# Performance work log

Hardware: AMD Instinct MI355X
Metric: run time of the kernel (lower is better)

Reference implementation:

```python
import jax, jax.numpy as jnp
import numpy as np

B, NPG, DEG = 16, 2048, 16          # graphs, nodes per graph, avg degree
N_TOT = B * NPG
E_TOT = N_TOT * DEG
NEG_SLOPE = 0.2


def _gat(x, src, dst, n, w, a_src, a_dst, b):
    # PyG GATConv: concat heads, add self loops, leaky_relu(0.2), segment softmax over targets
    H, C = a_src.shape
    h = (x @ w.T).reshape(n, H, C)                       # [n,H,C]
    sl = jnp.arange(n, dtype=src.dtype)
    s = jnp.concatenate([src, sl])
    d = jnp.concatenate([dst, sl])
    e = jax.nn.leaky_relu((h * a_src).sum(-1)[s] + (h * a_dst).sum(-1)[d], NEG_SLOPE)  # [E+n,H]
    emax = jax.lax.stop_gradient(jax.ops.segment_max(e, d, num_segments=n))
    ee = jnp.exp(e - emax[d])
    alpha = ee / (jax.ops.segment_sum(ee, d, num_segments=n)[d] + 1e-16)
    out = jax.ops.segment_sum(alpha[:, :, None] * h[s], d, num_segments=n)  # [n,H,C]
    return out.reshape(n, H * C) + b


def _gcn(x, src, dst, mask, n, w, b):
    # PyG GCNConv with self loops + symmetric norm; mask = float edge validity
    h = x @ w.T
    deg = jax.ops.segment_sum(mask, dst, num_segments=n) + 1.0  # +1 for self loop
    dinv = jax.lax.rsqrt(deg)
    coef = dinv[src] * dinv[dst] * mask
    out = jax.ops.segment_sum(coef[:, None] * h[src], dst, num_segments=n) + (dinv * dinv)[:, None] * h
    return out + b


def _sag(x, src, dst, mask, b_graphs, npg, k, w_rel, b_rel, w_root):
    # PyG SAGPooling(ratio=0.5): GraphConv score, per-graph top-k, x[perm]*tanh(score[perm]), filter_adj
    n = b_graphs * npg
    agg = jax.ops.segment_sum(mask[:, None] * x[src], dst, num_segments=n)
    score = (agg @ w_rel.T + b_rel + x @ w_root.T)[:, 0]      # [n]
    _, idx = jax.lax.top_k(score.reshape(b_graphs, npg), k)    # [B,k]
    perm = (jnp.arange(b_graphs, dtype=jnp.int32)[:, None] * npg + idx).reshape(-1)
    x_new = x[perm] * jnp.tanh(score[perm])[:, None]
    new_id = jnp.full((n,), -1, jnp.int32).at[perm].set(jnp.arange(b_graphs * k, dtype=jnp.int32))
    ns, nd = new_id[src], new_id[dst]
    valid = mask * ((ns >= 0) & (nd >= 0)).astype(x.dtype)
    return x_new, jnp.maximum(ns, 0), jnp.maximum(nd, 0), valid


def setup_inputs() -> dict:
    key = jax.random.key(0)
    ks = jax.random.split(key, 32)

    def lin(k, o, i):
        return (jax.random.normal(k, (o, i), jnp.float32) / np.sqrt(i)).astype(jnp.float32)

    x = jax.random.normal(ks[0], (N_TOT, 64), jnp.float32)
    off = jnp.repeat(jnp.arange(B, dtype=jnp.int32) * NPG, NPG * DEG)
    src = off + jax.random.randint(ks[1], (E_TOT,), 0, NPG, jnp.int32)
    dst = off + jax.random.randint(ks[2], (E_TOT,), 0, NPG, jnp.int32)
    edge_index = jnp.stack([src, dst])
    batch = jnp.repeat(jnp.arange(B, dtype=jnp.int32), NPG)

    return {
        'x': x, 'edge_index': edge_index, 'batch': batch,
        'gat1_w': lin(ks[3], 256, 64), 'gat1_asrc': lin(ks[4], 4, 64), 'gat1_adst': lin(ks[5], 4, 64),
        'gat1_b': jnp.zeros((256,), jnp.float32),
        'gat2_w': lin(ks[6], 256, 256), 'gat2_asrc': lin(ks[7], 4, 64), 'gat2_adst': lin(ks[8], 4, 64),
        'gat2_b': jnp.zeros((256,), jnp.float32),
        # pooling GCN1: 256 -> 128
        'gcn1_w': lin(ks[9], 128, 256), 'gcn1_b': jnp.zeros((128,), jnp.float32),
        'sag1_wrel': lin(ks[10], 1, 128), 'sag1_brel': jnp.zeros((1,), jnp.float32), 'sag1_wroot': lin(ks[11], 1, 128),
        # pooling GCN2: 128 -> 128
        'gcn2_w': lin(ks[12], 128, 128), 'gcn2_b': jnp.zeros((128,), jnp.float32),
        'sag2_wrel': lin(ks[13], 1, 128), 'sag2_brel': jnp.zeros((1,), jnp.float32), 'sag2_wroot': lin(ks[14], 1, 128),
        # classifier 128 -> 256 -> 128 -> 10
        'fc1_w': lin(ks[15], 256, 128), 'fc1_b': jnp.zeros((256,), jnp.float32),
        'fc2_w': lin(ks[16], 128, 256), 'fc2_b': jnp.zeros((128,), jnp.float32),
        'out_w': lin(ks[17], 10, 128), 'out_b': jnp.zeros((10,), jnp.float32),
    }


def reference(x, edge_index, batch,
              gat1_w, gat1_asrc, gat1_adst, gat1_b,
              gat2_w, gat2_asrc, gat2_adst, gat2_b,
              gcn1_w, gcn1_b, sag1_wrel, sag1_brel, sag1_wroot,
              gcn2_w, gcn2_b, sag2_wrel, sag2_brel, sag2_wroot,
              fc1_w, fc1_b, fc2_w, fc2_b, out_w, out_b):
    n = x.shape[0]
    src, dst = edge_index[0], edge_index[1]
    ones = jnp.ones(src.shape[0], x.dtype)

    # GAT encoder
    h = jax.nn.relu(_gat(x, src, dst, n, gat1_w, gat1_asrc, gat1_adst, gat1_b))
    h = _gat(h, src, dst, n, gat2_w, gat2_asrc, gat2_adst, gat2_b)  # [n,256]

    # GCN + SAGPool x2
    h = jax.nn.relu(_gcn(h, src, dst, ones, n, gcn1_w, gcn1_b))
    k1 = NPG // 2
    h, s1, d1, m1 = _sag(h, src, dst, ones, B, NPG, k1, sag1_wrel, sag1_brel, sag1_wroot)
    h = jax.nn.relu(_gcn(h, s1, d1, m1, B * k1, gcn2_w, gcn2_b))
    k2 = k1 // 2
    h, s2, d2, m2 = _sag(h, s1, d1, m1, B, k1, k2, sag2_wrel, sag2_brel, sag2_wroot)

    # global mean pool (equal-size graphs -> simple reshape-mean; batch vec implied)
    g = h.reshape(B, k2, -1).mean(axis=1)  # [B,128]

    # classifier MLP
    g = jax.nn.relu(g @ fc1_w.T + fc1_b)
    g = jax.nn.relu(g @ fc2_w.T + fc2_b)
    return g @ out_w.T + out_b  # [B,10]
```

## Files before the change

kernel.cpp:

```cpp
#include <hip/hip_runtime.h>

#define N1 32768
#define EE 524288
#define NB 16
#define DEG 16
#define NPG1 2048
#define KK1 1024
#define N2 16384
#define NPG2 1024
#define KK2 512
#define N3 8192
#define CAP 64

typedef _Float16 half8_t __attribute__((ext_vector_type(8)));
typedef float floatx16 __attribute__((ext_vector_type(16)));

static __device__ __forceinline__ float leaky(float x){ return fmaxf(x, 0.2f*x); }

__global__ void scatter_split(const int* __restrict__ src, const int* __restrict__ dst,
                              int* __restrict__ cnt, int* __restrict__ esrc,
                              const float* __restrict__ w0, int n0,
                              const float* __restrict__ w1, int n1,
                              const float* __restrict__ w2, int n2,
                              const float* __restrict__ w3, int n3,
                              _Float16* __restrict__ wh, _Float16* __restrict__ wl){
    int b = blockIdx.x;
    int tid = threadIdx.x;
    if (b < EE/256){
        int i = b*256 + tid;
        int d = dst[i];
        int p = atomicAdd(&cnt[d], 1);
        esrc[(d << 6) + p] = src[i];
    } else {
        int i = (b - EE/256)*256 + tid;
        int n01 = n0 + n1, n012 = n01 + n2, nt = n012 + n3;
        if (i >= nt) return;
        float v = (i < n0) ? w0[i] : (i < n01) ? w1[i - n0] : (i < n012) ? w2[i - n01] : w3[i - n012];
        _Float16 h = (_Float16)v;
        wh[i] = h; wl[i] = (_Float16)(v - (float)h);
    }
}

__global__ void csr2_build(const int* __restrict__ perm, const int* __restrict__ nid,
                           const int* __restrict__ cnt, const int* __restrict__ EL,
                           int2* __restrict__ rpx2, float* __restrict__ dinv2,
                           int* __restrict__ EL2){
    int lane = threadIdx.x & 63;
    int w = threadIdx.x >> 6;
    int d2 = blockIdx.x*4 + w;
    int old = __builtin_amdgcn_readfirstlane(perm[d2]);
    int beg = old << 6;
    int end = beg + cnt[old];
    unsigned long long below = (1ull << lane) - 1ull;
    int c2 = 0;
    for (int i = beg; i < end; i += 64){
        int ii = i + lane;
        int sn = -1;
        if (ii < end) sn = nid[EL[ii]];
        bool take = sn >= 0;
        unsigned long long m = __ballot(take);
        int pos = c2 + __popcll(m & below);
        if (take) EL2[beg + pos] = sn;
        c2 += __popcll(m);
    }
    if (lane == 0){
        rpx2[d2] = make_int2(beg, beg + c2);
        dinv2[d2] = rsqrtf((float)c2 + 1.0f);
    }
}

#define KS 64
static __device__ __forceinline__ int ldsoff(int row, int k8){
    return row*64 + ((k8 ^ (row & 7)) << 3);
}

__global__ __launch_bounds__(256, 2) void gemm_h2(const float* __restrict__ A,
        const _Float16* __restrict__ WHp, const _Float16* __restrict__ WLp,
        float* __restrict__ C, int n, int K, int M,
        const int* __restrict__ perm, const float* __restrict__ tt,
        const float* __restrict__ asrc, const float* __restrict__ adst,
        float* __restrict__ AS, float* __restrict__ AD){
    __shared__ _Float16 sm[4*128*KS];
    _Float16* sAH = sm;
    _Float16* sAL = sm + 128*KS;
    _Float16* sWH = sm + 2*128*KS;
    _Float16* sWL = sm + 3*128*KS;
    int t = threadIdx.x;
    int lane = t & 63;
    int wid = t >> 6;
    int wr = wid >> 1, wc = wid & 1;
    int row0 = blockIdx.x*128, col0 = blockIdx.y*128;
    int srow = t >> 3;
    int sk8  = t & 7;

    floatx16 acc[2][2];
    #pragma unroll
    for (int i = 0; i < 2; i++)
        #pragma unroll
        for (int j = 0; j < 2; j++)
            #pragma unroll
            for (int q = 0; q < 16; q++) acc[i][j][q] = 0.f;

    for (int kk = 0; kk < K; kk += KS){
        #pragma unroll
        for (int p = 0; p < 4; p++){
            int r = srow + p*32;
            int rr = row0 + r;
            int arow = perm ? perm[rr] : rr;
            float tscale = perm ? tt[rr] : 1.0f;
            const float* ga = A + (size_t)arow*K + kk + sk8*8;
            float4 a0 = *(const float4*)ga;
            float4 a1 = *(const float4*)(ga + 4);
            half8_t ahi, alo;
            float av[8] = {a0.x,a0.y,a0.z,a0.w,a1.x,a1.y,a1.z,a1.w};
            #pragma unroll
            for (int q = 0; q < 8; q++){
                float v = av[q] * tscale;
                _Float16 h = (_Float16)v;
                ahi[q] = h; alo[q] = (_Float16)(v - (float)h);
            }
            size_t wo = (size_t)(col0 + r)*K + kk + sk8*8;
            half8_t whi = *(const half8_t*)(WHp + wo);
            half8_t wlo = *(const half8_t*)(WLp + wo);
            int o = ldsoff(r, sk8);
            *(half8_t*)&sAH[o] = ahi;
            *(half8_t*)&sAL[o] = alo;
            *(half8_t*)&sWH[o] = whi;
            *(half8_t*)&sWL[o] = wlo;
        }
        __syncthreads();
        #pragma unroll
        for (int kc = 0; kc < 4; kc++){
            int k8 = kc*2 + (lane >> 5);
            int ra = wr*64 + (lane & 31);
            int rb = wc*64 + (lane & 31);
            half8_t ah0 = *(const half8_t*)&sAH[ldsoff(ra,      k8)];
            half8_t ah1 = *(const half8_t*)&sAH[ldsoff(ra + 32, k8)];
            half8_t al0 = *(const half8_t*)&sAL[ldsoff(ra,      k8)];
            half8_t al1 = *(const half8_t*)&sAL[ldsoff(ra + 32, k8)];
            half8_t bh0 = *(const half8_t*)&sWH[ldsoff(rb,      k8)];
            half8_t bh1 = *(const half8_t*)&sWH[ldsoff(rb + 32, k8)];
            half8_t bl0 = *(const half8_t*)&sWL[ldsoff(rb,      k8)];
            half8_t bl1 = *(const half8_t*)&sWL[ldsoff(rb + 32, k8)];
            acc[0][0] = __builtin_amdgcn_mfma_f32_32x32x16_f16(ah0, bh0, acc[0][0], 0,0,0);
            acc[0][0] = __builtin_amdgcn_mfma_f32_32x32x16_f16(ah0, bl0, acc[0][0], 0,0,0);
            acc[0][0] = __builtin_amdgcn_mfma_f32_32x32x16_f16(al0, bh0, acc[0][0], 0,0,0);
            acc[0][1] = __builtin_amdgcn_mfma_f32_32x32x16_f16(ah0, bh1, acc[0][1], 0,0,0);
            acc[0][1] = __builtin_amdgcn_mfma_f32_32x32x16_f16(ah0, bl1, acc[0][1], 0,0,0);
            acc[0][1] = __builtin_amdgcn_mfma_f32_32x32x16_f16(al0, bh1, acc[0][1], 0,0,0);
            acc[1][0] = __builtin_amdgcn_mfma_f32_32x32x16_f16(ah1, bh0, acc[1][0], 0,0,0);
            acc[1][0] = __builtin_amdgcn_mfma_f32_32x32x16_f16(ah1, bl0, acc[1][0], 0,0,0);
            acc[1][0] = __builtin_amdgcn_mfma_f32_32x32x16_f16(al1, bh0, acc[1][0], 0,0,0);
            acc[1][1] = __builtin_amdgcn_mfma_f32_32x32x16_f16(ah1, bh1, acc[1][1], 0,0,0);
            acc[1][1] = __builtin_amdgcn_mfma_f32_32x32x16_f16(ah1, bl1, acc[1][1], 0,0,0);
            acc[1][1] = __builtin_amdgcn_mfma_f32_32x32x16_f16(al1, bh1, acc[1][1], 0,0,0);
        }
        __syncthreads();
    }
    #pragma unroll
    for (int rt = 0; rt < 2; rt++)
        #pragma unroll
        for (int ct = 0; ct < 2; ct++){
            int baser = row0 + wr*64 + rt*32 + 4*(lane >> 5);
            int c = col0 + wc*64 + ct*32 + (lane & 31);
            #pragma unroll
            for (int r = 0; r < 16; r++){
                int rr = baser + (r & 3) + 8*(r >> 2);
                C[(size_t)rr*M + c] = acc[rt][ct][r];
            }
        }
    if (asrc){
        int hh = (col0 >> 6) + wc;
        float a_s0 = asrc[col0 + wc*64 +  0 + (lane & 31)];
        float a_s1 = asrc[col0 + wc*64 + 32 + (lane & 31)];
        float a_d0 = adst[col0 + wc*64 +  0 + (lane & 31)];
        float a_d1 = adst[col0 + wc*64 + 32 + (lane & 31)];
        #pragma unroll
        for (int rt = 0; rt < 2; rt++){
            floatx16 vs, vd;
            #pragma unroll
            for (int r = 0; r < 16; r++){
                vs[r] = acc[rt][0][r]*a_s0 + acc[rt][1][r]*a_s1;
                vd[r] = acc[rt][0][r]*a_d0 + acc[rt][1][r]*a_d1;
            }
            #pragma unroll
            for (int off = 1; off < 32; off <<= 1){
                #pragma unroll
                for (int r = 0; r < 16; r++){
                    vs[r] += __shfl_xor(vs[r], off);
                    vd[r] += __shfl_xor(vd[r], off);
                }
            }
            if ((lane & 31) == 0){
                int baser = row0 + wr*64 + rt*32 + 4*(lane >> 5);
                #pragma unroll
                for (int r = 0; r < 16; r++){
                    int rr = baser + (r & 3) + 8*(r >> 2);
                    AS[rr*4 + hh] = vs[r];
                    AD[rr*4 + hh] = vd[r];
                }
            }
        }
    }
}

template<int RELU>
__global__ void gat_agg(const float* __restrict__ h, const float* __restrict__ as_,
                        const float* __restrict__ ad_, const float* __restrict__ bias,
                        const int* __restrict__ cnt, const int* __restrict__ esrc,
                        float* __restrict__ out){
    int lane = threadIdx.x & 63;
    int nb = gridDim.x;
    int b = blockIdx.x;
    int sb = (b & 7)*(nb >> 3) + (b >> 3);
    int d = __builtin_amdgcn_readfirstlane(sb*4 + (int)(threadIdx.x >> 6));
    int beg = d << 6;
    int end = beg + cnt[d];

    int hh = lane >> 4;
    float adh = ad_[(d<<2) + hh];
    float aself = as_[(d<<2) + hh];

    float dn[4];
    dn[0] = __expf(leaky(aself + adh)); dn[1] = 0.f; dn[2] = 0.f; dn[3] = 0.f;
    float4 hd = ((const float4*)(h + ((size_t)d<<8)))[lane];
    float4 AX[4];
    AX[0].x = dn[0]*hd.x; AX[0].y = dn[0]*hd.y; AX[0].z = dn[0]*hd.z; AX[0].w = dn[0]*hd.w;
    AX[1] = {0,0,0,0}; AX[2] = {0,0,0,0}; AX[3] = {0,0,0,0};

    int i = beg;
    int endu = beg + ((end - beg) & ~7);
    for (; i < endu; i += 8){
        int s_[8];
        #pragma unroll
        for (int j = 0; j < 8; j++) s_[j] = __builtin_amdgcn_readfirstlane(esrc[i + j]);
        float a_[8];
        #pragma unroll
        for (int j = 0; j < 8; j++) a_[j] = as_[(s_[j]<<2) + hh];
        float4 hv_[8];
        #pragma unroll
        for (int j = 0; j < 8; j++) hv_[j] = ((const float4*)(h + ((size_t)s_[j]<<8)))[lane];
        #pragma unroll
        for (int j = 0; j < 8; j++){
            float x = a_[j] + adh;
            float p = __expf(fmaxf(x, 0.2f*x));
            dn[j & 3] += p;
            AX[j & 3].x = fmaf(p, hv_[j].x, AX[j & 3].x);
            AX[j & 3].y = fmaf(p, hv_[j].y, AX[j & 3].y);
            AX[j & 3].z = fmaf(p, hv_[j].z, AX[j & 3].z);
            AX[j & 3].w = fmaf(p, hv_[j].w, AX[j & 3].w);
        }
    }
    for (; i < end; ++i){
        int s = __builtin_amdgcn_readfirstlane(esrc[i]);
        float x = as_[(s<<2) + hh] + adh;
        float4 hv = ((const float4*)(h + ((size_t)s<<8)))[lane];
        float p = __expf(fmaxf(x, 0.2f*x));
        dn[0] += p;
        AX[0].x = fmaf(p, hv.x, AX[0].x); AX[0].y = fmaf(p, hv.y, AX[0].y);
        AX[0].z = fmaf(p, hv.z, AX[0].z); AX[0].w = fmaf(p, hv.w, AX[0].w);
    }
    float den = ((dn[0] + dn[1]) + (dn[2] + dn[3])) + 1e-16f;
    float r = 1.0f / den;
    int c0 = lane*4;
    float4 bv = *(const float4*)(bias + c0);
    float4 acc;
    acc.x = ((AX[0].x+AX[1].x)+(AX[2].x+AX[3].x))*r + bv.x;
    acc.y = ((AX[0].y+AX[1].y)+(AX[2].y+AX[3].y))*r + bv.y;
    acc.z = ((AX[0].z+AX[1].z)+(AX[2].z+AX[3].z))*r + bv.z;
    acc.w = ((AX[0].w+AX[1].w)+(AX[2].w+AX[3].w))*r + bv.w;
    if (RELU){
        acc.x = fmaxf(acc.x, 0.f); acc.y = fmaxf(acc.y, 0.f);
        acc.z = fmaxf(acc.z, 0.f); acc.w = fmaxf(acc.w, 0.f);
    }
    ((float4*)(out + ((size_t)d<<8)))[lane] = acc;
}

template<int MODE>
__global__ void gcn_agg_sag(const float* __restrict__ h, const int* __restrict__ cnt,
                            const int2* __restrict__ rpx, const float* __restrict__ dinv,
                            const float* __restrict__ bias,
                            const float* __restrict__ wrel, const float* __restrict__ wroot,
                            const float* __restrict__ brel,
                            const int* __restrict__ esrc,
                            float* __restrict__ out, float* __restrict__ Y, float* __restrict__ Z){
    int lane = threadIdx.x & 63;
    int nb = gridDim.x;
    int b = blockIdx.x;
    int sb = (b & 7)*(nb >> 3) + (b >> 3);
    int d = __builtin_amdgcn_readfirstlane(sb*4 + (int)(threadIdx.x >> 6));
    int beg, end;
    float dv;
    if (MODE == 0){
        beg = d << 6; end = beg + cnt[d];
        dv = rsqrtf((float)(end - beg) + 1.0f);
    } else {
        int2 re = rpx[d]; beg = re.x; end = re.y;
        dv = dinv[d];
    }
    int c0 = lane*2;
    float2 hd = ((const float2*)(h + ((size_t)d<<7)))[lane];
    float self = dv*dv;
    float ax[4] = {self*hd.x, 0.f, 0.f, 0.f};
    float ay[4] = {self*hd.y, 0.f, 0.f, 0.f};
    int i = beg;
    int endu = beg + ((end - beg) & ~7);
    for (; i < endu; i += 8){
        int s_[8];
        #pragma unroll
        for (int j = 0; j < 8; j++) s_[j] = __builtin_amdgcn_readfirstlane(esrc[i + j]);
        float di_[8];
        #pragma unroll
        for (int j = 0; j < 8; j++){
            if (MODE == 0) di_[j] = rsqrtf((float)cnt[s_[j]] + 1.0f);
            else           di_[j] = dinv[s_[j]];
        }
        float2 hv_[8];
        #pragma unroll
        for (int j = 0; j < 8; j++) hv_[j] = ((const float2*)(h + ((size_t)s_[j]<<7)))[lane];
        #pragma unroll
        for (int j = 0; j < 8; j++){
            float coef = di_[j]*dv;
            ax[j & 3] = fmaf(coef, hv_[j].x, ax[j & 3]);
            ay[j & 3] = fmaf(coef, hv_[j].y, ay[j & 3]);
        }
    }
    for (; i < end; ++i){
        int s = __builtin_amdgcn_readfirstlane(esrc[i]);
        float di = (MODE == 0) ? rsqrtf((float)cnt[s] + 1.0f) : dinv[s];
        float coef = di*dv;
        float2 hv = ((const float2*)(h + ((size_t)s<<7)))[lane];
        ax[0] = fmaf(coef, hv.x, ax[0]); ay[0] = fmaf(coef, hv.y, ay[0]);
    }
    float axs = ((ax[0]+ax[1])+(ax[2]+ax[3]));
    float ays = ((ay[0]+ay[1])+(ay[2]+ay[3]));
    axs = fmaxf(axs + bias[c0], 0.f);
    ays = fmaxf(ays + bias[c0+1], 0.f);
    float2 o; o.x = axs; o.y = ays;
    ((float2*)(out + ((size_t)d<<7)))[lane] = o;
    float py = axs*wrel[c0]  + ays*wrel[c0+1];
    float pz = axs*wroot[c0] + ays*wroot[c0+1];
    #pragma unroll
    for (int off = 32; off; off >>= 1){ py += __shfl_xor(py, off); pz += __shfl_xor(pz, off); }
    if (lane == 0){ Y[d] = py; Z[d] = pz + brel[0]; }
}

template<int MODE>
__global__ void sag_lite(const float* __restrict__ Y, const float* __restrict__ Z,
                         const int* __restrict__ cnt, const int2* __restrict__ rpx,
                         const int* __restrict__ esrc, float* __restrict__ score){
    int lane = threadIdx.x & 63;
    int w = threadIdx.x >> 6;
    int nb = gridDim.x;
    int b = blockIdx.x;
    int sb = (b & 7)*(nb >> 3) + (b >> 3);
    int d = sb*4 + w;
    int beg, end;
    if (MODE == 0){ beg = d << 6; end = beg + cnt[d]; }
    else { int2 re = rpx[d]; beg = re.x; end = re.y; }
    float s = 0.f;
    for (int i = beg + lane; i < end; i += 64) s += Y[esrc[i]];
    #pragma unroll
    for (int off = 32; off; off >>= 1) s += __shfl_xor(s, off);
    if (lane == 0) score[d] = s + Z[d];
}

__global__ __launch_bounds__(64) void topk_wave(const float* __restrict__ score,
        int npg, int k, int* __restrict__ perm, float* __restrict__ ssort,
        int* __restrict__ nid, int writeNid){
    __shared__ unsigned keys[2048];
    __shared__ int hist[256];
    int g = blockIdx.x;
    int lane = threadIdx.x;
    int nch = npg >> 6;
    for (int c = 0; c < nch; c++){
        unsigned u = __float_as_uint(score[g*npg + c*64 + lane]);
        keys[c*64 + lane] = (u & 0x80000000u) ? ~u : (u | 0x80000000u);
    }
    int need = k;
    unsigned prefix = 0u, pmask = 0u;
    #pragma unroll
    for (int shift = 24; shift >= 0; shift -= 8){
        #pragma unroll
        for (int q = 0; q < 4; q++) hist[lane*4 + q] = 0;
        for (int c = 0; c < nch; c++){
            unsigned u = keys[c*64 + lane];
            if ((u & pmask) == prefix) atomicAdd(&hist[(u >> shift) & 255u], 1);
        }
        int h0 = hist[lane*4], h1 = hist[lane*4+1], h2 = hist[lane*4+2], h3 = hist[lane*4+3];
        int s3 = h3, s2 = h2 + s3, s1 = h1 + s2, s0 = h0 + s1;
        int tot = s0;
        int suf = tot;
        #pragma unroll
        for (int off = 1; off < 64; off <<= 1){
            int v = __shfl_down(suf, off);
            if (lane + off < 64) suf += v;
        }
        int above_quad = suf - tot;
        int c0 = s0 + above_quad, c1 = s1 + above_quad, c2 = s2 + above_quad, c3 = s3 + above_quad;
        int sel = -1;
        if (c0 >= need && c1 < need) sel = 0;
        if (c1 >= need && c2 < need) sel = 1;
        if (c2 >= need && c3 < need) sel = 2;
        if (c3 >= need && above_quad < need) sel = 3;
        unsigned long long msk = __ballot(sel >= 0);
        int srcl = __ffsll((long long)msk) - 1;
        int binq = __shfl(sel, srcl);
        int bin = srcl*4 + binq;
        int cge_next = (binq == 0) ? __shfl(c1, srcl) :
                       (binq == 1) ? __shfl(c2, srcl) :
                       (binq == 2) ? __shfl(c3, srcl) : __shfl(above_quad, srcl);
        need -= cge_next;
        prefix |= ((unsigned)bin) << shift;
        pmask  |= 255u << shift;
    }
    unsigned thr = prefix;
    int m = need;
    unsigned long long below = (1ull << lane) - 1ull;
    int base = 0, eqbase = 0;
    for (int c = 0; c < nch; c++){
        unsigned u = keys[c*64 + lane];
        bool gt = u > thr;
        bool eq = (u == thr);
        unsigned long long meq = __ballot(eq);
        int eqrank = eqbase + __popcll(meq & below);
        bool take = gt || (eq && eqrank < m);
        unsigned long long mtk = __ballot(take);
        int pos = base + __popcll(mtk & below);
        int node = g*npg + c*64 + lane;
        if (take){
            perm[g*k + pos] = node;
            ssort[g*k + pos] = tanhf(score[node]);
            if (writeNid) nid[node] = g*k + pos;
        } else if (writeNid) nid[node] = -1;
        base += __popcll(mtk);
        eqbase += __popcll(meq);
    }
}

__global__ void pool_mlp(const float* __restrict__ x, const int* __restrict__ perm,
                         const float* __restrict__ ssort,
                         const float* __restrict__ fc1w, const float* __restrict__ fc1b,
                         const float* __restrict__ fc2w, const float* __restrict__ fc2b,
                         const float* __restrict__ ow,  const float* __restrict__ ob,
                         float* __restrict__ out){
    __shared__ float tt[KK2];
    __shared__ float part[128];
    __shared__ float gv[128], t1[256], t2[128];
    int b = blockIdx.x, t = threadIdx.x;
    tt[t]       = ssort[b*KK2 + t];
    tt[t + 256] = ssort[b*KK2 + t + 256];
    __syncthreads();
    int c = t & 127, half = t >> 7;
    float s = 0.f;
    #pragma unroll 4
    for (int i = half*256; i < half*256 + 256; i++){
        int o = perm[b*KK2 + i];
        s = fmaf(tt[i], x[(size_t)o*128 + c], s);
    }
    if (half) part[c] = s;
    __syncthreads();
    if (!half) gv[c] = (s + part[c]) * (1.0f/KK2);
    __syncthreads();
    {
        float s1 = fc1b[t];
        for (int cc = 0; cc < 128; cc++) s1 += gv[cc]*fc1w[t*128 + cc];
        t1[t] = fmaxf(s1, 0.f);
    }
    __syncthreads();
    if (t < 128){
        float s2 = fc2b[t];
        for (int cc = 0; cc < 256; cc++) s2 += t1[cc]*fc2w[t*256 + cc];
        t2[t] = fmaxf(s2, 0.f);
    }
    __syncthreads();
    if (t < 10){
        float s3 = ob[t];
        for (int cc = 0; cc < 128; cc++) s3 += t2[cc]*ow[t*128 + cc];
        out[b*10 + t] = s3;
    }
}

extern "C" void kernel_launch(void* const* d_in, const int* in_sizes, int n_in,
                              void* d_out, int out_size, void* d_ws, size_t ws_size,
                              hipStream_t stream){
    (void)in_sizes; (void)n_in; (void)out_size; (void)ws_size;
    const float* x    = (const float*)d_in[0];
    const int*   eidx = (const int*)d_in[1];
    const int*   src  = eidx;
    const int*   dst  = eidx + EE;
    const float* g1w  = (const float*)d_in[3];
    const float* g1as = (const float*)d_in[4];
    const float* g1ad = (const float*)d_in[5];
    const float* g1b  = (const float*)d_in[6];
    const float* g2w  = (const float*)d_in[7];
    const float* g2as = (const float*)d_in[8];
    const float* g2ad = (const float*)d_in[9];
    const float* g2b  = (const float*)d_in[10];
    const float* c1w  = (const float*)d_in[11];
    const float* c1b  = (const float*)d_in[12];
    const float* s1wrel  = (const float*)d_in[13];
    const float* s1brel  = (const float*)d_in[14];
    const float* s1wroot = (const float*)d_in[15];
    const float* c2w  = (const float*)d_in[16];
    const float* c2b  = (const float*)d_in[17];
    const float* s2wrel  = (const float*)d_in[18];
    const float* s2brel  = (const float*)d_in[19];
    const float* s2wroot = (const float*)d_in[20];
    const float* f1w  = (const float*)d_in[21];
    const float* f1b  = (const float*)d_in[22];
    const float* f2w  = (const float*)d_in[23];
    const float* f2b  = (const float*)d_in[24];
    const float* ow   = (const float*)d_in[25];
    const float* ob   = (const float*)d_in[26];
    float* out = (float*)d_out;

    char* ws = (char*)d_ws;
    size_t off = 0;
    auto alloc = [&](size_t bytes)->char*{
        char* p = ws + off;
        off += (bytes + 255) & ~(size_t)255;
        return p;
    };
    float* F0     = (float*)alloc((size_t)N1*256*4);
    float* F1     = (float*)alloc((size_t)N1*256*4);
    float* F2     = (float*)alloc((size_t)N2*128*4);
    float* AS     = (float*)alloc((size_t)N1*4*4);
    float* AD     = (float*)alloc((size_t)N1*4*4);
    int*   CNT    = (int*)  alloc((size_t)N1*4);
    int*   EL     = (int*)  alloc((size_t)N1*CAP*4);
    float* SCORE  = (float*)alloc((size_t)N1*4);
    float* Y      = (float*)alloc((size_t)N1*4);
    float* Z      = (float*)alloc((size_t)N1*4);
    int*   PERM1  = (int*)  alloc((size_t)N2*4);
    float* SSORT1 = (float*)alloc((size_t)N2*4);
    int*   NID    = (int*)  alloc((size_t)N1*4);
    int2*  RPX2   = (int2*) alloc((size_t)N2*8);
    int*   EL2    = (int*)  alloc((size_t)N1*CAP*4);
    float* DINV2  = (float*)alloc((size_t)N2*4);
    int*   PERM2  = (int*)  alloc((size_t)N3*4);
    float* SSORT2 = (float*)alloc((size_t)N3*4);
    _Float16* WH  = (_Float16*)alloc((size_t)131072*2);
    _Float16* WL  = (_Float16*)alloc((size_t)131072*2);
    const int o_g1 = 0, o_g2 = 16384, o_c1 = 81920, o_c2 = 114688;

    hipMemsetAsync(CNT, 0, (size_t)N1*4, stream);
    scatter_split<<<EE/256 + 512, 256, 0, stream>>>(src, dst, CNT, EL,
        g1w, 16384, g2w, 65536, c1w, 32768, c2w, 16384, WH, WL);

    gemm_h2<<<dim3(N1/128, 2), 256, 0, stream>>>(x, WH + o_g1, WL + o_g1, F0, N1, 64, 256,
                                                 nullptr, nullptr, g1as, g1ad, AS, AD);
    gat_agg<1><<<N1/4, 256, 0, stream>>>(F0, AS, AD, g1b, CNT, EL, F1);

    gemm_h2<<<dim3(N1/128, 2), 256, 0, stream>>>(F1, WH + o_g2, WL + o_g2, F0, N1, 256, 256,
                                                 nullptr, nullptr, g2as, g2ad, AS, AD);
    gat_agg<0><<<N1/4, 256, 0, stream>>>(F0, AS, AD, g2b, CNT, EL, F1);

    gemm_h2<<<dim3(N1/128, 1), 256, 0, stream>>>(F1, WH + o_c1, WL + o_c1, F0, N1, 256, 128,
                                                 nullptr, nullptr, nullptr, nullptr, nullptr, nullptr);
    gcn_agg_sag<0><<<N1/4, 256, 0, stream>>>(F0, CNT, nullptr, nullptr, c1b,
                                             s1wrel, s1wroot, s1brel, EL, F1, Y, Z);

    sag_lite<0><<<N1/4, 256, 0, stream>>>(Y, Z, CNT, nullptr, EL, SCORE);
    topk_wave<<<NB, 64, 0, stream>>>(SCORE, NPG1, KK1, PERM1, SSORT1, NID, 1);

    csr2_build<<<N2/4, 256, 0, stream>>>(PERM1, NID, CNT, EL, RPX2, DINV2, EL2);

    gemm_h2<<<dim3(N2/128, 1), 256, 0, stream>>>(F1, WH + o_c2, WL + o_c2, F0, N2, 128, 128,
                                                 PERM1, SSORT1, nullptr, nullptr, nullptr, nullptr);
    gcn_agg_sag<1><<<N2/4, 256, 0, stream>>>(F0, nullptr, RPX2, DINV2, c2b,
                                             s2wrel, s2wroot, s2brel, EL2, F2, Y, Z);

    sag_lite<1><<<N2/4, 256, 0, stream>>>(Y, Z, nullptr, RPX2, EL2, SCORE);
    topk_wave<<<NB, 64, 0, stream>>>(SCORE, NPG2, KK2, PERM2, SSORT2, nullptr, 0);

    pool_mlp<<<NB, 256, 0, stream>>>(F2, PERM2, SSORT2,
                                     f1w, f1b, f2w, f2b, ow, ob, out);
}
```

Measured before the change: 289.6 us.

## Halve GEMM row tile and split GAT aggregation across two waves per node

The GEMM now uses 64-row tiles instead of 128, with each wave computing one 32-row slab. Shared memory drops to 48 KB and launch bounds rise to 3 blocks per CU, so there are twice as many blocks and higher occupancy. The GAT aggregation assigns two waves per destination node, each handling 128 channels with float2 loads, which doubles the number of waves issuing gathers. The trade-off is less reuse of the W tile per block, more redundant W loads from global memory, and duplicated edge-index and attention-score reads across the two half-waves.

```diff
diff --git a/kernel.cpp b/kernel.cpp
--- a/kernel.cpp
+++ b/kernel.cpp
@@ -74,36 +74,32 @@
     return row*64 + ((k8 ^ (row & 7)) << 3);
 }
 
-__global__ __launch_bounds__(256, 2) void gemm_h2(const float* __restrict__ A,
+__global__ __launch_bounds__(256, 3) void gemm_h2(const float* __restrict__ A,
         const _Float16* __restrict__ WHp, const _Float16* __restrict__ WLp,
         float* __restrict__ C, int n, int K, int M,
         const int* __restrict__ perm, const float* __restrict__ tt,
         const float* __restrict__ asrc, const float* __restrict__ adst,
         float* __restrict__ AS, float* __restrict__ AD){
-    __shared__ _Float16 sm[4*128*KS];
+    __shared__ _Float16 sm[384*KS];
     _Float16* sAH = sm;
-    _Float16* sAL = sm + 128*KS;
-    _Float16* sWH = sm + 2*128*KS;
-    _Float16* sWL = sm + 3*128*KS;
+    _Float16* sAL = sm + 64*KS;
+    _Float16* sWH = sm + 128*KS;
+    _Float16* sWL = sm + 256*KS;
     int t = threadIdx.x;
     int lane = t & 63;
     int wid = t >> 6;
     int wr = wid >> 1, wc = wid & 1;
-    int row0 = blockIdx.x*128, col0 = blockIdx.y*128;
+    int row0 = blockIdx.x*64, col0 = blockIdx.y*128;
     int srow = t >> 3;
     int sk8  = t & 7;
 
-    floatx16 acc[2][2];
+    floatx16 acc[2];
     #pragma unroll
-    for (int i = 0; i < 2; i++)
-        #pragma unroll
-        for (int j = 0; j < 2; j++)
-            #pragma unroll
-            for (int q = 0; q < 16; q++) acc[i][j][q] = 0.f;
+    for (int q = 0; q < 16; q++){ acc[0][q] = 0.f; acc[1][q] = 0.f; }
 
     for (int kk = 0; kk < K; kk += KS){
         #pragma unroll
-        for (int p = 0; p < 4; p++){
+        for (int p = 0; p < 2; p++){
             int r = srow + p*32;
             int rr = row0 + r;
             int arow = perm ? perm[rr] : rr;
@@ -119,12 +115,17 @@
                 _Float16 h = (_Float16)v;
                 ahi[q] = h; alo[q] = (_Float16)(v - (float)h);
             }
+            int o = ldsoff(r, sk8);
+            *(half8_t*)&sAH[o] = ahi;
+            *(half8_t*)&sAL[o] = alo;
+        }
+        #pragma unroll
+        for (int p = 0; p < 4; p++){
+            int r = srow + p*32;
             size_t wo = (size_t)(col0 + r)*K + kk + sk8*8;
             half8_t whi = *(const half8_t*)(WHp + wo);
             half8_t wlo = *(const half8_t*)(WLp + wo);
             int o = ldsoff(r, sk8);
-            *(half8_t*)&sAH[o] = ahi;
-            *(half8_t*)&sAL[o] = alo;
             *(half8_t*)&sWH[o] = whi;
             *(half8_t*)&sWL[o] = wlo;
         }
@@ -132,73 +133,60 @@
         #pragma unroll
         for (int kc = 0; kc < 4; kc++){
             int k8 = kc*2 + (lane >> 5);
-            int ra = wr*64 + (lane & 31);
+            int ra = wr*32 + (lane & 31);
             int rb = wc*64 + (lane & 31);
-            half8_t ah0 = *(const half8_t*)&sAH[ldsoff(ra,      k8)];
-            half8_t ah1 = *(const half8_t*)&sAH[ldsoff(ra + 32, k8)];
-            half8_t al0 = *(const half8_t*)&sAL[ldsoff(ra,      k8)];
-            half8_t al1 = *(const half8_t*)&sAL[ldsoff(ra + 32, k8)];
+            half8_t ah  = *(const half8_t*)&sAH[ldsoff(ra, k8)];
+            half8_t al  = *(const half8_t*)&sAL[ldsoff(ra, k8)];
             half8_t bh0 = *(const half8_t*)&sWH[ldsoff(rb,      k8)];
             half8_t bh1 = *(const half8_t*)&sWH[ldsoff(rb + 32, k8)];
             half8_t bl0 = *(const half8_t*)&sWL[ldsoff(rb,      k8)];
             half8_t bl1 = *(const half8_t*)&sWL[ldsoff(rb + 32, k8)];
-            acc[0][0] = __builtin_amdgcn_mfma_f32_32x32x16_f16(ah0, bh0, acc[0][0], 0,0,0);
-            acc[0][0] = __builtin_amdgcn_mfma_f32_32x32x16_f16(ah0, bl0, acc[0][0], 0,0,0);
-            acc[0][0] = __builtin_amdgcn_mfma_f32_32x32x16_f16(al0, bh0, acc[0][0], 0,0,0);
-            acc[0][1] = __builtin_amdgcn_mfma_f32_32x32x16_f16(ah0, bh1, acc[0][1], 0,0,0);
-            acc[0][1] = __builtin_amdgcn_mfma_f32_32x32x16_f16(ah0, bl1, acc[0][1], 0,0,0);
-            acc[0][1] = __builtin_amdgcn_mfma_f32_32x32x16_f16(al0, bh1, acc[0][1], 0,0,0);
-            acc[1][0] = __builtin_amdgcn_mfma_f32_32x32x16_f16(ah1, bh0, acc[1][0], 0,0,0);
-            acc[1][0] = __builtin_amdgcn_mfma_f32_32x32x16_f16(ah1, bl0, acc[1][0], 0,0,0);
-            acc[1][0] = __builtin_amdgcn_mfma_f32_32x32x16_f16(al1, bh0, acc[1][0], 0,0,0);
-            acc[1][1] = __builtin_amdgcn_mfma_f32_32x32x16_f16(ah1, bh1, acc[1][1], 0,0,0);
-            acc[1][1] = __builtin_amdgcn_mfma_f32_32x32x16_f16(ah1, bl1, acc[1][1], 0,0,0);
-            acc[1][1] = __builtin_amdgcn_mfma_f32_32x32x16_f16(al1, bh1, acc[1][1], 0,0,0);
+            acc[0] = __builtin_amdgcn_mfma_f32_32x32x16_f16(ah, bh0, acc[0], 0,0,0);
+            acc[0] = __builtin_amdgcn_mfma_f32_32x32x16_f16(ah, bl0, acc[0], 0,0,0);
+            acc[0] = __builtin_amdgcn_mfma_f32_32x32x16_f16(al, bh0, acc[0], 0,0,0);
+            acc[1] = __builtin_amdgcn_mfma_f32_32x32x16_f16(ah, bh1, acc[1], 0,0,0);
+            acc[1] = __builtin_amdgcn_mfma_f32_32x32x16_f16(ah, bl1, acc[1], 0,0,0);
+            acc[1] = __builtin_amdgcn_mfma_f32_32x32x16_f16(al, bh1, acc[1], 0,0,0);
         }
         __syncthreads();
     }
     #pragma unroll
-    for (int rt = 0; rt < 2; rt++)
-        #pragma unroll
-        for (int ct = 0; ct < 2; ct++){
-            int baser = row0 + wr*64 + rt*32 + 4*(lane >> 5);
-            int c = col0 + wc*64 + ct*32 + (lane & 31);
-            #pragma unroll
-            for (int r = 0; r < 16; r++){
-                int rr = baser + (r & 3) + 8*(r >> 2);
-                C[(size_t)rr*M + c] = acc[rt][ct][r];
-            }
-        }
+    for (int ct = 0; ct < 2; ct++){
+        int baser = row0 + wr*32 + 4*(lane >> 5);
+        int c = col0 + wc*64 + ct*32 + (lane & 31);
+        #pragma unroll
+        for (int r = 0; r < 16; r++){
+            int rr = baser + (r & 3) + 8*(r >> 2);
+            C[(size_t)rr*M + c] = acc[ct][r];
+        }
+    }
     if (asrc){
         int hh = (col0 >> 6) + wc;
         float a_s0 = asrc[col0 + wc*64 +  0 + (lane & 31)];
         float a_s1 = asrc[col0 + wc*64 + 32 + (lane & 31)];
         float a_d0 = adst[col0 + wc*64 +  0 + (lane & 31)];
         float a_d1 = adst[col0 + wc*64 + 32 + (lane & 31)];
-        #pragma unroll
-        for (int rt = 0; rt < 2; rt++){
-            floatx16 vs, vd;
+        floatx16 vs, vd;
+        #pragma unroll
+        for (int r = 0; r < 16; r++){
+            vs[r] = acc[0][r]*a_s0 + acc[1][r]*a_s1;
+            vd[r] = acc[0][r]*a_d0 + acc[1][r]*a_d1;
+        }
+        #pragma unroll
+        for (int off = 1; off < 32; off <<= 1){
             #pragma unroll
             for (int r = 0; r < 16; r++){
-                vs[r] = acc[rt][0][r]*a_s0 + acc[rt][1][r]*a_s1;
-                vd[r] = acc[rt][0][r]*a_d0 + acc[rt][1][r]*a_d1;
+                vs[r] += __shfl_xor(vs[r], off);
+                vd[r] += __shfl_xor(vd[r], off);
             }
+        }
+        if ((lane & 31) == 0){
+            int baser = row0 + wr*32 + 4*(lane >> 5);
             #pragma unroll
-            for (int off = 1; off < 32; off <<= 1){
-                #pragma unroll
-                for (int r = 0; r < 16; r++){
-                    vs[r] += __shfl_xor(vs[r], off);
-                    vd[r] += __shfl_xor(vd[r], off);
-                }
-            }
-            if ((lane & 31) == 0){
-                int baser = row0 + wr*64 + rt*32 + 4*(lane >> 5);
-                #pragma unroll
-                for (int r = 0; r < 16; r++){
-                    int rr = baser + (r & 3) + 8*(r >> 2);
-                    AS[rr*4 + hh] = vs[r];
-                    AD[rr*4 + hh] = vd[r];
-                }
+            for (int r = 0; r < 16; r++){
+                int rr = baser + (r & 3) + 8*(r >> 2);
+                AS[rr*4 + hh] = vs[r];
+                AD[rr*4 + hh] = vd[r];
             }
         }
     }
@@ -210,23 +198,26 @@
                         const int* __restrict__ cnt, const int* __restrict__ esrc,
                         float* __restrict__ out){
     int lane = threadIdx.x & 63;
+    int wid = threadIdx.x >> 6;
     int nb = gridDim.x;
     int b = blockIdx.x;
     int sb = (b & 7)*(nb >> 3) + (b >> 3);
-    int d = __builtin_amdgcn_readfirstlane(sb*4 + (int)(threadIdx.x >> 6));
+    int d = __builtin_amdgcn_readfirstlane(sb*2 + (wid >> 1));
+    int half = wid & 1;
     int beg = d << 6;
     int end = beg + cnt[d];
 
-    int hh = lane >> 4;
+    int c0 = half*128 + lane*2;
+    int hh = c0 >> 6;
     float adh = ad_[(d<<2) + hh];
     float aself = as_[(d<<2) + hh];
 
     float dn[4];
     dn[0] = __expf(leaky(aself + adh)); dn[1] = 0.f; dn[2] = 0.f; dn[3] = 0.f;
-    float4 hd = ((const float4*)(h + ((size_t)d<<8)))[lane];
-    float4 AX[4];
-    AX[0].x = dn[0]*hd.x; AX[0].y = dn[0]*hd.y; AX[0].z = dn[0]*hd.z; AX[0].w = dn[0]*hd.w;
-    AX[1] = {0,0,0,0}; AX[2] = {0,0,0,0}; AX[3] = {0,0,0,0};
+    float2 hd = *(const float2*)(h + ((size_t)d<<8) + c0);
+    float2 AX[4];
+    AX[0].x = dn[0]*hd.x; AX[0].y = dn[0]*hd.y;
+    AX[1] = {0,0}; AX[2] = {0,0}; AX[3] = {0,0};
 
     int i = beg;
     int endu = beg + ((end - beg) & ~7);
@@ -237,9 +228,9 @@
         float a_[8];
         #pragma unroll
         for (int j = 0; j < 8; j++) a_[j] = as_[(s_[j]<<2) + hh];
-        float4 hv_[8];
-        #pragma unroll
-        for (int j = 0; j < 8; j++) hv_[j] = ((const float4*)(h + ((size_t)s_[j]<<8)))[lane];
+        float2 hv_[8];
+        #pragma unroll
+        for (int j = 0; j < 8; j++) hv_[j] = *(const float2*)(h + ((size_t)s_[j]<<8) + c0);
         #pragma unroll
         for (int j = 0; j < 8; j++){
             float x = a_[j] + adh;
@@ -247,33 +238,26 @@
             dn[j & 3] += p;
             AX[j & 3].x = fmaf(p, hv_[j].x, AX[j & 3].x);
             AX[j & 3].y = fmaf(p, hv_[j].y, AX[j & 3].y);
-            AX[j & 3].z = fmaf(p, hv_[j].z, AX[j & 3].z);
-            AX[j & 3].w = fmaf(p, hv_[j].w, AX[j & 3].w);
         }
     }
     for (; i < end; ++i){
         int s = __builtin_amdgcn_readfirstlane(esrc[i]);
         float x = as_[(s<<2) + hh] + adh;
-        float4 hv = ((const float4*)(h + ((size_t)s<<8)))[lane];
+        float2 hv = *(const float2*)(h + ((size_t)s<<8) + c0);
         float p = __expf(fmaxf(x, 0.2f*x));
         dn[0] += p;
         AX[0].x = fmaf(p, hv.x, AX[0].x); AX[0].y = fmaf(p, hv.y, AX[0].y);
-        AX[0].z = fmaf(p, hv.z, AX[0].z); AX[0].w = fmaf(p, hv.w, AX[0].w);
     }
     float den = ((dn[0] + dn[1]) + (dn[2] + dn[3])) + 1e-16f;
     float r = 1.0f / den;
-    int c0 = lane*4;
-    float4 bv = *(const float4*)(bias + c0);
-    float4 acc;
+    float2 bv = *(const float2*)(bias + c0);
+    float2 acc;
     acc.x = ((AX[0].x+AX[1].x)+(AX[2].x+AX[3].x))*r + bv.x;
     acc.y = ((AX[0].y+AX[1].y)+(AX[2].y+AX[3].y))*r + bv.y;
-    acc.z = ((AX[0].z+AX[1].z)+(AX[2].z+AX[3].z))*r + bv.z;
-    acc.w = ((AX[0].w+AX[1].w)+(AX[2].w+AX[3].w))*r + bv.w;
     if (RELU){
         acc.x = fmaxf(acc.x, 0.f); acc.y = fmaxf(acc.y, 0.f);
-        acc.z = fmaxf(acc.z, 0.f); acc.w = fmaxf(acc.w, 0.f);
-    }
-    ((float4*)(out + ((size_t)d<<8)))[lane] = acc;
+    }
+    *(float2*)(out + ((size_t)d<<8) + c0) = acc;
 }
 
 template<int MODE>
@@ -548,16 +532,16 @@
     scatter_split<<<EE/256 + 512, 256, 0, stream>>>(src, dst, CNT, EL,
         g1w, 16384, g2w, 65536, c1w, 32768, c2w, 16384, WH, WL);
 
-    gemm_h2<<<dim3(N1/128, 2), 256, 0, stream>>>(x, WH + o_g1, WL + o_g1, F0, N1, 64, 256,
-                                                 nullptr, nullptr, g1as, g1ad, AS, AD);
-    gat_agg<1><<<N1/4, 256, 0, stream>>>(F0, AS, AD, g1b, CNT, EL, F1);
-
-    gemm_h2<<<dim3(N1/128, 2), 256, 0, stream>>>(F1, WH + o_g2, WL + o_g2, F0, N1, 256, 256,
-                                                 nullptr, nullptr, g2as, g2ad, AS, AD);
-    gat_agg<0><<<N1/4, 256, 0, stream>>>(F0, AS, AD, g2b, CNT, EL, F1);
-
-    gemm_h2<<<dim3(N1/128, 1), 256, 0, stream>>>(F1, WH + o_c1, WL + o_c1, F0, N1, 256, 128,
-                                                 nullptr, nullptr, nullptr, nullptr, nullptr, nullptr);
+    gemm_h2<<<dim3(N1/64, 2), 256, 0, stream>>>(x, WH + o_g1, WL + o_g1, F0, N1, 64, 256,
+                                                nullptr, nullptr, g1as, g1ad, AS, AD);
+    gat_agg<1><<<N1/2, 256, 0, stream>>>(F0, AS, AD, g1b, CNT, EL, F1);
+
+    gemm_h2<<<dim3(N1/64, 2), 256, 0, stream>>>(F1, WH + o_g2, WL + o_g2, F0, N1, 256, 256,
+                                                nullptr, nullptr, g2as, g2ad, AS, AD);
+    gat_agg<0><<<N1/2, 256, 0, stream>>>(F0, AS, AD, g2b, CNT, EL, F1);
+
+    gemm_h2<<<dim3(N1/64, 1), 256, 0, stream>>>(F1, WH + o_c1, WL + o_c1, F0, N1, 256, 128,
+                                                nullptr, nullptr, nullptr, nullptr, nullptr, nullptr);
     gcn_agg_sag<0><<<N1/4, 256, 0, stream>>>(F0, CNT, nullptr, nullptr, c1b,
                                              s1wrel, s1wroot, s1brel, EL, F1, Y, Z);
 
@@ -566,8 +550,8 @@
 
     csr2_build<<<N2/4, 256, 0, stream>>>(PERM1, NID, CNT, EL, RPX2, DINV2, EL2);
 
-    gemm_h2<<<dim3(N2/128, 1), 256, 0, stream>>>(F1, WH + o_c2, WL + o_c2, F0, N2, 128, 128,
-                                                 PERM1, SSORT1, nullptr, nullptr, nullptr, nullptr);
+    gemm_h2<<<dim3(N2/64, 1), 256, 0, stream>>>(F1, WH + o_c2, WL + o_c2, F0, N2, 128, 128,
+                                                PERM1, SSORT1, nullptr, nullptr, nullptr, nullptr);
     gcn_agg_sag<1><<<N2/4, 256, 0, stream>>>(F0, nullptr, RPX2, DINV2, c2b,
                                              s2wrel, s2wroot, s2brel, EL2, F2, Y, Z);
 
```

Result: slower. 325.1 us (+12.2%).
